# Kernel tuning notes

Hardware: AMD Instinct MI355X
Metric: run time of the kernel (lower is better)

Reference implementation:

```python
import jax, jax.numpy as jnp
import numpy as np

N = 50000        # nodes
E = 150000       # edges (avg degree ~3, chain-like RNA graphs)
F_IN = 32        # n_features
H = 32           # hidden_dim
C = 13           # n_classes
L = 3            # n_conv_layers
EDGE_HID = 10    # edge-net hidden width (Linear(2,10))
BN_EPS = 1e-5
SLOPE = 0.01     # leaky_relu default negative slope


def setup_inputs() -> dict:
    key = jax.random.key(0)
    ks = jax.random.split(key, 8)
    s = 0.1
    x = jax.random.normal(ks[0], (N, F_IN), dtype=jnp.float32)
    edge_index = jax.random.randint(ks[1], (2, E), 0, N)
    edge_attr = jax.random.uniform(ks[2], (E, 2), dtype=jnp.float32)
    # per-layer NNConv params stacked on a leading L axis (F_IN == H so all layers share shapes)
    netW1 = jax.random.normal(ks[3], (L, 2, EDGE_HID), dtype=jnp.float32) * s
    netb1 = jnp.zeros((L, EDGE_HID), dtype=jnp.float32)
    netW2 = jax.random.normal(ks[4], (L, EDGE_HID, F_IN * H), dtype=jnp.float32) * (s / np.sqrt(EDGE_HID).astype(np.float32))
    netb2 = jnp.zeros((L, F_IN * H), dtype=jnp.float32)
    root = jax.random.normal(ks[5], (L, F_IN, H), dtype=jnp.float32) * s
    conv_bias = jnp.zeros((L, H), dtype=jnp.float32)
    bn_gamma = jnp.ones((L, H), dtype=jnp.float32)
    bn_beta = jnp.zeros((L, H), dtype=jnp.float32)
    fcW = jax.random.normal(ks[6], (H, C), dtype=jnp.float32) * s
    fcb = jnp.zeros((C,), dtype=jnp.float32)
    return {"x": x, "edge_index": edge_index, "edge_attr": edge_attr,
            "netW1": netW1, "netb1": netb1, "netW2": netW2, "netb2": netb2,
            "root": root, "conv_bias": conv_bias,
            "bn_gamma": bn_gamma, "bn_beta": bn_beta, "fcW": fcW, "fcb": fcb}


def reference(x, edge_index, edge_attr, netW1, netb1, netW2, netb2, root,
              conv_bias, bn_gamma, bn_beta, fcW, fcb):
    src, dst = edge_index[0], edge_index[1]
    n = x.shape[0]
    h = x
    for i in range(L):
        # NNConv: per-edge weight matrix from edge MLP
        e = jax.nn.relu(edge_attr @ netW1[i] + netb1[i])            # [E, EDGE_HID]
        w = (e @ netW2[i] + netb2[i]).reshape(-1, h.shape[1], H)    # [E, in, H]
        m = jnp.einsum('ei,eio->eo', h[src], w)                     # messages [E, H]
        agg = jax.ops.segment_sum(m, dst, num_segments=n)           # scatter-add to targets
        h = agg + h @ root[i] + conv_bias[i]
        # BatchNorm1d (training-mode batch statistics)
        mu = h.mean(axis=0)
        var = h.var(axis=0)
        h = (h - mu) * jax.lax.rsqrt(var + BN_EPS) * bn_gamma[i] + bn_beta[i]
        # leaky_relu; dropout=0 is identity
        h = jnp.where(h > 0, h, SLOPE * h)
    logits = h @ fcW + fcb
    return jax.nn.log_softmax(logits, axis=1)
```

## Files before the change

### kernel.cpp

```cpp
#include <hip/hip_runtime.h>

#define NN 50000
#define EE 150000
#define BN_EPS 1e-5f
#define SLOPE 0.01f
#define SCAN_B 196
#define AGG_B  782
#define MSG_B  2344
#define CAP    344

typedef __attribute__((ext_vector_type(8))) short bf16x8;
typedef __attribute__((ext_vector_type(4))) float f32x4;

__global__ __launch_bounds__(256) void k_count(const int* __restrict__ ei, int* __restrict__ cnt) {
    int e = blockIdx.x * blockDim.x + threadIdx.x;
    if (e < EE) atomicAdd(&cnt[ei[EE + e]], 1);
}

__global__ __launch_bounds__(256) void k_scanA(const int* __restrict__ cnt,
                                               int* __restrict__ rowptr,
                                               int* __restrict__ bsum) {
    __shared__ int buf[256];
    int t = threadIdx.x;
    int idx = blockIdx.x * 256 + t;
    int v = (idx <= NN) ? cnt[idx] : 0;
    buf[t] = v;
    __syncthreads();
    for (int off = 1; off < 256; off <<= 1) {
        int add = (t >= off) ? buf[t - off] : 0;
        __syncthreads();
        buf[t] += add;
        __syncthreads();
    }
    if (idx <= NN) rowptr[idx] = buf[t] - v;
    if (t == 255) bsum[blockIdx.x] = buf[255];
}

__global__ __launch_bounds__(256) void k_scanB(int* __restrict__ bsum) {
    __shared__ int buf[256];
    int t = threadIdx.x;
    int v = (t < SCAN_B) ? bsum[t] : 0;
    buf[t] = v;
    __syncthreads();
    for (int off = 1; off < 256; off <<= 1) {
        int add = (t >= off) ? buf[t - off] : 0;
        __syncthreads();
        buf[t] += add;
        __syncthreads();
    }
    if (t < SCAN_B) bsum[t] = buf[t] - v;
}

__global__ __launch_bounds__(256) void k_scanC(int* __restrict__ rowptr,
                                               int* __restrict__ cursor,
                                               const int* __restrict__ bsum) {
    int idx = blockIdx.x * 256 + threadIdx.x;
    if (idx <= NN) {
        int r = rowptr[idx] + bsum[blockIdx.x];
        rowptr[idx] = r;
        cursor[idx] = r;
    }
}

__global__ __launch_bounds__(256) void k_fill(const int* __restrict__ ei,
                                              int* __restrict__ cursor,
                                              int* __restrict__ perm) {
    int e = blockIdx.x * blockDim.x + threadIdx.x;
    if (e < EE) perm[e] = atomicAdd(&cursor[ei[EE + e]], 1);
}

__global__ __launch_bounds__(256) void k_wprep(const float* __restrict__ netW2,
                                               const float* __restrict__ netb2,
                                               unsigned* __restrict__ Wfz) {
    int layer = blockIdx.y;
    int idx = blockIdx.x * 256 + threadIdx.x;
    if (idx >= 5632) return;
    const float* W2 = netW2 + layer * 10240;
    const float* b2 = netb2 + layer * 1024;
    int frag = idx >> 8;
    int rem  = idx & 255;
    int lane = rem >> 2;
    int j0   = (rem & 3) * 2;
    int tile = frag & 1;
    int kstep = frag >> 1;
    int o  = tile * 16 + (lane & 15);
    int kk = kstep * 32 + (lane >> 4) * 8 + j0;
    float v0, v1;
    if (kk < 320) {
        int base = (kk >> 5) * 1024 + (kk & 31) * 32 + o;
        v0 = W2[base];
        v1 = W2[base + 32];
    } else {
        int base = (kk - 320) * 32 + o;
        v0 = b2[base];
        v1 = b2[base + 32];
    }
    Wfz[layer * 5632 + idx] =
        __builtin_amdgcn_perm(__float_as_uint(v1), __float_as_uint(v0), 0x07060302u);
}

__device__ __forceinline__ void bn_scsh(const float* __restrict__ stats,
                                        const float* __restrict__ gamma,
                                        const float* __restrict__ beta,
                                        int flag, float* sc, float* sh) {
    if (flag && threadIdx.x < 32) {
        int o = threadIdx.x;
        float mu = stats[o] * (1.0f / NN);
        float var = stats[32 + o] * (1.0f / NN) - mu * mu;
        float s = gamma[o] * rsqrtf(var + BN_EPS);
        sc[o] = s;
        sh[o] = fmaf(-mu, s, beta[o]);
    }
}

__global__ __launch_bounds__(256) void k_msg(
    const float* __restrict__ h, const int* __restrict__ ei,
    const float* __restrict__ ea, const float* __restrict__ W1,
    const float* __restrict__ b1, const unsigned* __restrict__ Wfz,
    const float* __restrict__ stats, const float* __restrict__ gamma,
    const float* __restrict__ beta, int flag,
    const int* __restrict__ perm, float* __restrict__ m)
{
    int t = threadIdx.x;
    int lane = t & 63;
    int w = t >> 6;
    int col = lane & 15;
    int chunk = lane >> 4;
    int e = blockIdx.x * 64 + w * 16 + col;
    bool ev = e < EE;
    int s = ev ? ei[e] : 0;
    float2 a = ev ? ((const float2*)ea)[e] : make_float2(0.f, 0.f);

    float hv[8];
    *(float4*)&hv[0] = *(const float4*)(h + s * 32 + chunk * 8);
    *(float4*)&hv[4] = *(const float4*)(h + s * 32 + chunk * 8 + 4);

    if (flag) {
        int i0 = chunk * 8;
#pragma unroll
        for (int j = 0; j < 8; ++j) {
            int ch = i0 + j;
            float mu = stats[ch] * (1.0f / NN);
            float var = stats[32 + ch] * (1.0f / NN) - mu * mu;
            float scv = gamma[ch] * rsqrtf(var + BN_EPS);
            float shv = fmaf(-mu, scv, beta[ch]);
            float y = fmaf(hv[j], scv, shv);
            hv[j] = y > 0.f ? y : SLOPE * y;
        }
    }

    float ekv[11];
#pragma unroll
    for (int k = 0; k < 10; ++k)
        ekv[k] = fmaxf(fmaf(a.x, W1[k], fmaf(a.y, W1[10 + k], b1[k])), 0.0f);
    ekv[10] = 1.0f;

    f32x4 acc0 = {0.f, 0.f, 0.f, 0.f};
    f32x4 acc1 = {0.f, 0.f, 0.f, 0.f};
#pragma unroll
    for (int k = 0; k < 11; ++k) {
        float ekk = ekv[k];
        union { unsigned u[4]; bf16x8 v; } B;
        B.u[0] = __builtin_amdgcn_perm(__float_as_uint(ekk * hv[1]), __float_as_uint(ekk * hv[0]), 0x07060302u);
        B.u[1] = __builtin_amdgcn_perm(__float_as_uint(ekk * hv[3]), __float_as_uint(ekk * hv[2]), 0x07060302u);
        B.u[2] = __builtin_amdgcn_perm(__float_as_uint(ekk * hv[5]), __float_as_uint(ekk * hv[4]), 0x07060302u);
        B.u[3] = __builtin_amdgcn_perm(__float_as_uint(ekk * hv[7]), __float_as_uint(ekk * hv[6]), 0x07060302u);
        bf16x8 A0 = *(const bf16x8*)(Wfz + (k * 2)     * 256 + lane * 4);
        bf16x8 A1 = *(const bf16x8*)(Wfz + (k * 2 + 1) * 256 + lane * 4);
        acc0 = __builtin_amdgcn_mfma_f32_16x16x32_bf16(A0, B.v, acc0, 0, 0, 0);
        acc1 = __builtin_amdgcn_mfma_f32_16x16x32_bf16(A1, B.v, acc1, 0, 0, 0);
    }

    if (ev) {
        int p = perm[e];
        int r = chunk * 4;
        *(f32x4*)(m + (size_t)p * 32 + r)      = acc0;
        *(f32x4*)(m + (size_t)p * 32 + 16 + r) = acc1;
    }
}

__global__ __launch_bounds__(512) void k_agg(
    const float* __restrict__ h, const float* __restrict__ m,
    const int* __restrict__ rowptr,
    const float* __restrict__ root, const float* __restrict__ bias,
    const float* __restrict__ stats_prev, const float* __restrict__ gamma,
    const float* __restrict__ beta, int flag,
    float* __restrict__ hpre, float* __restrict__ stats_out)
{
    __shared__ float smb[CAP * 36];
    __shared__ float sc[32], sh[32];
    __shared__ float ls[2][8][8][4];

    bn_scsh(stats_prev, gamma, beta, flag, sc, sh);

    int t = threadIdx.x;
    int v0 = blockIdx.x * 64;
    int vend = v0 + 64 < NN ? v0 + 64 : NN;
    int p_start = rowptr[v0];
    int span = rowptr[vend] - p_start;
    int nstage = span < CAP ? span : CAP;

    for (int idx = t; idx < nstage * 8; idx += 512) {
        int r = idx >> 3, j = idx & 7;
        *(float4*)&smb[r * 36 + j * 4] = ((const float4*)m)[(size_t)(p_start + r) * 8 + j];
    }
    __syncthreads();

    int v = v0 + (t >> 3);
    int cg = t & 7;
    float4 acc = make_float4(0.f, 0.f, 0.f, 0.f);

    if (v < NN) {
        float hn[32];
        const float4* hp = (const float4*)(h + v * 32);
#pragma unroll
        for (int q = 0; q < 8; ++q) {
            float4 tt = hp[q];
            hn[4 * q] = tt.x; hn[4 * q + 1] = tt.y; hn[4 * q + 2] = tt.z; hn[4 * q + 3] = tt.w;
        }
        if (flag) {
#pragma unroll
            for (int i = 0; i < 32; ++i) {
                float y = fmaf(hn[i], sc[i], sh[i]);
                hn[i] = y > 0.f ? y : SLOPE * y;
            }
        }
        acc = ((const float4*)bias)[cg];
#pragma unroll
        for (int i = 0; i < 32; ++i) {
            float4 r = ((const float4*)(root + i * 32))[cg];
            acc.x = fmaf(hn[i], r.x, acc.x);
            acc.y = fmaf(hn[i], r.y, acc.y);
            acc.z = fmaf(hn[i], r.z, acc.z);
            acc.w = fmaf(hn[i], r.w, acc.w);
        }
        int q0 = rowptr[v] - p_start, q1 = rowptr[v + 1] - p_start;
        for (int p = q0; p < q1; ++p) {
            float4 tt;
            if (p < CAP) tt = *(const float4*)&smb[p * 36 + cg * 4];
            else         tt = ((const float4*)m)[(size_t)(p_start + p) * 8 + cg];
            acc.x += tt.x; acc.y += tt.y; acc.z += tt.z; acc.w += tt.w;
        }
        ((float4*)(hpre + v * 32))[cg] = acc;
    }

    float ss[8] = { acc.x, acc.y, acc.z, acc.w,
                    acc.x * acc.x, acc.y * acc.y, acc.z * acc.z, acc.w * acc.w };
#pragma unroll
    for (int d = 8; d < 64; d <<= 1) {
#pragma unroll
        for (int j = 0; j < 8; ++j) ss[j] += __shfl_xor(ss[j], d);
    }
    int wave = t >> 6, lane = t & 63;
    if (lane < 8) {
#pragma unroll
        for (int j = 0; j < 4; ++j) {
            ls[0][wave][lane][j] = ss[j];
            ls[1][wave][lane][j] = ss[4 + j];
        }
    }
    __syncthreads();
    if (t < 64) {
        int stat = t >> 5, idx = t & 31;
        int cgg = idx >> 2, ch = idx & 3;
        float val = 0.f;
#pragma unroll
        for (int wv = 0; wv < 8; ++wv) val += ls[stat][wv][cgg][ch];
        unsafeAtomicAdd(&stats_out[stat * 32 + idx], val);
    }
}

__global__ __launch_bounds__(256) void k_logits(const float* __restrict__ h,
                                                const float* __restrict__ fcW,
                                                const float* __restrict__ fcb,
                                                const float* __restrict__ stats,
                                                const float* __restrict__ gamma,
                                                const float* __restrict__ beta,
                                                float* __restrict__ out) {
    __shared__ float sc[32], sh[32];
    bn_scsh(stats, gamma, beta, 1, sc, sh);
    __syncthreads();

    int v = blockIdx.x * blockDim.x + threadIdx.x;
    if (v >= NN) return;
    float hv[32];
    const float4* hp = (const float4*)(h + v * 32);
#pragma unroll
    for (int q = 0; q < 8; ++q) {
        float4 t = hp[q];
        hv[4 * q] = t.x; hv[4 * q + 1] = t.y; hv[4 * q + 2] = t.z; hv[4 * q + 3] = t.w;
    }
#pragma unroll
    for (int i = 0; i < 32; ++i) {
        float y = fmaf(hv[i], sc[i], sh[i]);
        hv[i] = y > 0.f ? y : SLOPE * y;
    }
    float lg[13];
#pragma unroll
    for (int c = 0; c < 13; ++c) lg[c] = fcb[c];
#pragma unroll
    for (int i = 0; i < 32; ++i) {
        float z = hv[i];
#pragma unroll
        for (int c = 0; c < 13; ++c) lg[c] = fmaf(z, fcW[i * 13 + c], lg[c]);
    }
    float mx = lg[0];
#pragma unroll
    for (int c = 1; c < 13; ++c) mx = fmaxf(mx, lg[c]);
    float sum = 0.0f;
#pragma unroll
    for (int c = 0; c < 13; ++c) sum += expf(lg[c] - mx);
    float lse = mx + logf(sum);
#pragma unroll
    for (int c = 0; c < 13; ++c) out[v * 13 + c] = lg[c] - lse;
}

extern "C" void kernel_launch(void* const* d_in, const int* in_sizes, int n_in,
                              void* d_out, int out_size, void* d_ws, size_t ws_size,
                              hipStream_t stream) {
    const float* x     = (const float*)d_in[0];
    const int*   ei    = (const int*)  d_in[1];
    const float* ea    = (const float*)d_in[2];
    const float* netW1 = (const float*)d_in[3];
    const float* netb1 = (const float*)d_in[4];
    const float* netW2 = (const float*)d_in[5];
    const float* netb2 = (const float*)d_in[6];
    const float* root  = (const float*)d_in[7];
    const float* cbias = (const float*)d_in[8];
    const float* gamma = (const float*)d_in[9];
    const float* beta  = (const float*)d_in[10];
    const float* fcW   = (const float*)d_in[11];
    const float* fcb   = (const float*)d_in[12];
    float* out = (float*)d_out;

    char* w = (char*)d_ws;
    float*    m      = (float*)   (w);
    float*    hA     = (float*)   (w + 19200000);
    float*    hB     = (float*)   (w + 25600000);
    int*      rowptr = (int*)     (w + 32000000);
    int*      cursor = (int*)     (w + 32200064);
    int*      perm   = (int*)     (w + 32400128);
    float*    stats  = (float*)   (w + 33000128);
    int*      bsum   = (int*)     (w + 33000896);
    unsigned* Wfz    = (unsigned*)(w + 33001920);
    int*      cnt    = (int*)w;

    hipMemsetAsync(cnt, 0, (NN + 1) * sizeof(int), stream);
    hipMemsetAsync(stats, 0, 768, stream);

    k_wprep<<<dim3(22, 3), 256, 0, stream>>>(netW2, netb2, Wfz);
    k_count<<<(EE + 255) / 256, 256, 0, stream>>>(ei, cnt);
    k_scanA<<<SCAN_B, 256, 0, stream>>>(cnt, rowptr, bsum);
    k_scanB<<<1, 256, 0, stream>>>(bsum);
    k_scanC<<<SCAN_B, 256, 0, stream>>>(rowptr, cursor, bsum);
    k_fill <<<(EE + 255) / 256, 256, 0, stream>>>(ei, cursor, perm);

    const float* hcur = x;
    float* bufs[2] = { hA, hB };
    for (int i = 0; i < 3; ++i) {
        float* hnext = bufs[i & 1];
        const float* stprev = stats + (i - 1) * 64;
        k_msg<<<MSG_B, 256, 0, stream>>>(
            hcur, ei, ea, netW1 + i * 20, netb1 + i * 10, Wfz + i * 5632,
            stprev, gamma + (i - 1) * 32, beta + (i - 1) * 32, i > 0, perm, m);
        k_agg<<<AGG_B, 512, 0, stream>>>(
            hcur, m, rowptr, root + i * 1024, cbias + i * 32,
            stprev, gamma + (i - 1) * 32, beta + (i - 1) * 32, i > 0,
            hnext, stats + i * 64);
        hcur = hnext;
    }
    k_logits<<<(NN + 255) / 256, 256, 0, stream>>>(
        hcur, fcW, fcb, stats + 2 * 64, gamma + 2 * 32, beta + 2 * 32, out);
}
```

Before: 257.4 us.

## Fuse message computation into aggregation kernel via dst-sorted edge ids

Replaces the separate per-edge message kernel and per-node aggregation kernel with one per-layer kernel. Each block handles 64 destination nodes, walks their incoming edges through a dst-sorted edge-id list, computes messages with MFMA straight into shared memory in CAP-sized chunks, then reduces them. This removes the global round-trip of the E×32 message buffer and one launch per layer. In exchange the edge work is tied to the node blocking, which adds a barrier per chunk, gives uneven work across blocks, and reads h[src] and edge data indirectly through eids.

```diff
diff --git a/kernel.cpp b/kernel.cpp
--- a/kernel.cpp
+++ b/kernel.cpp
@@ -6,7 +6,6 @@
 #define SLOPE 0.01f
 #define SCAN_B 196
 #define AGG_B  782
-#define MSG_B  2344
 #define CAP    344
 
 typedef __attribute__((ext_vector_type(8))) short bf16x8;
@@ -64,9 +63,12 @@
 
 __global__ __launch_bounds__(256) void k_fill(const int* __restrict__ ei,
                                               int* __restrict__ cursor,
-                                              int* __restrict__ perm) {
+                                              int* __restrict__ eids) {
     int e = blockIdx.x * blockDim.x + threadIdx.x;
-    if (e < EE) perm[e] = atomicAdd(&cursor[ei[EE + e]], 1);
+    if (e < EE) {
+        int pos = atomicAdd(&cursor[ei[EE + e]], 1);
+        eids[pos] = e;
+    }
 }
 
 __global__ __launch_bounds__(256) void k_wprep(const float* __restrict__ netW2,
@@ -113,75 +115,11 @@
     }
 }
 
-__global__ __launch_bounds__(256) void k_msg(
+__global__ __launch_bounds__(512) void k_layer(
     const float* __restrict__ h, const int* __restrict__ ei,
     const float* __restrict__ ea, const float* __restrict__ W1,
     const float* __restrict__ b1, const unsigned* __restrict__ Wfz,
-    const float* __restrict__ stats, const float* __restrict__ gamma,
-    const float* __restrict__ beta, int flag,
-    const int* __restrict__ perm, float* __restrict__ m)
-{
-    int t = threadIdx.x;
-    int lane = t & 63;
-    int w = t >> 6;
-    int col = lane & 15;
-    int chunk = lane >> 4;
-    int e = blockIdx.x * 64 + w * 16 + col;
-    bool ev = e < EE;
-    int s = ev ? ei[e] : 0;
-    float2 a = ev ? ((const float2*)ea)[e] : make_float2(0.f, 0.f);
-
-    float hv[8];
-    *(float4*)&hv[0] = *(const float4*)(h + s * 32 + chunk * 8);
-    *(float4*)&hv[4] = *(const float4*)(h + s * 32 + chunk * 8 + 4);
-
-    if (flag) {
-        int i0 = chunk * 8;
-#pragma unroll
-        for (int j = 0; j < 8; ++j) {
-            int ch = i0 + j;
-            float mu = stats[ch] * (1.0f / NN);
-            float var = stats[32 + ch] * (1.0f / NN) - mu * mu;
-            float scv = gamma[ch] * rsqrtf(var + BN_EPS);
-            float shv = fmaf(-mu, scv, beta[ch]);
-            float y = fmaf(hv[j], scv, shv);
-            hv[j] = y > 0.f ? y : SLOPE * y;
-        }
-    }
-
-    float ekv[11];
-#pragma unroll
-    for (int k = 0; k < 10; ++k)
-        ekv[k] = fmaxf(fmaf(a.x, W1[k], fmaf(a.y, W1[10 + k], b1[k])), 0.0f);
-    ekv[10] = 1.0f;
-
-    f32x4 acc0 = {0.f, 0.f, 0.f, 0.f};
-    f32x4 acc1 = {0.f, 0.f, 0.f, 0.f};
-#pragma unroll
-    for (int k = 0; k < 11; ++k) {
-        float ekk = ekv[k];
-        union { unsigned u[4]; bf16x8 v; } B;
-        B.u[0] = __builtin_amdgcn_perm(__float_as_uint(ekk * hv[1]), __float_as_uint(ekk * hv[0]), 0x07060302u);
-        B.u[1] = __builtin_amdgcn_perm(__float_as_uint(ekk * hv[3]), __float_as_uint(ekk * hv[2]), 0x07060302u);
-        B.u[2] = __builtin_amdgcn_perm(__float_as_uint(ekk * hv[5]), __float_as_uint(ekk * hv[4]), 0x07060302u);
-        B.u[3] = __builtin_amdgcn_perm(__float_as_uint(ekk * hv[7]), __float_as_uint(ekk * hv[6]), 0x07060302u);
-        bf16x8 A0 = *(const bf16x8*)(Wfz + (k * 2)     * 256 + lane * 4);
-        bf16x8 A1 = *(const bf16x8*)(Wfz + (k * 2 + 1) * 256 + lane * 4);
-        acc0 = __builtin_amdgcn_mfma_f32_16x16x32_bf16(A0, B.v, acc0, 0, 0, 0);
-        acc1 = __builtin_amdgcn_mfma_f32_16x16x32_bf16(A1, B.v, acc1, 0, 0, 0);
-    }
-
-    if (ev) {
-        int p = perm[e];
-        int r = chunk * 4;
-        *(f32x4*)(m + (size_t)p * 32 + r)      = acc0;
-        *(f32x4*)(m + (size_t)p * 32 + 16 + r) = acc1;
-    }
-}
-
-__global__ __launch_bounds__(512) void k_agg(
-    const float* __restrict__ h, const float* __restrict__ m,
-    const int* __restrict__ rowptr,
+    const int* __restrict__ rowptr, const int* __restrict__ eids,
     const float* __restrict__ root, const float* __restrict__ bias,
     const float* __restrict__ stats_prev, const float* __restrict__ gamma,
     const float* __restrict__ beta, int flag,
@@ -191,20 +129,14 @@
     __shared__ float sc[32], sh[32];
     __shared__ float ls[2][8][8][4];
 
+    int t = threadIdx.x;
     bn_scsh(stats_prev, gamma, beta, flag, sc, sh);
-
-    int t = threadIdx.x;
+    __syncthreads();
+
     int v0 = blockIdx.x * 64;
     int vend = v0 + 64 < NN ? v0 + 64 : NN;
     int p_start = rowptr[v0];
     int span = rowptr[vend] - p_start;
-    int nstage = span < CAP ? span : CAP;
-
-    for (int idx = t; idx < nstage * 8; idx += 512) {
-        int r = idx >> 3, j = idx & 7;
-        *(float4*)&smb[r * 36 + j * 4] = ((const float4*)m)[(size_t)(p_start + r) * 8 + j];
-    }
-    __syncthreads();
 
     int v = v0 + (t >> 3);
     int cg = t & 7;
@@ -234,15 +166,78 @@
             acc.z = fmaf(hn[i], r.z, acc.z);
             acc.w = fmaf(hn[i], r.w, acc.w);
         }
-        int q0 = rowptr[v] - p_start, q1 = rowptr[v + 1] - p_start;
-        for (int p = q0; p < q1; ++p) {
-            float4 tt;
-            if (p < CAP) tt = *(const float4*)&smb[p * 36 + cg * 4];
-            else         tt = ((const float4*)m)[(size_t)(p_start + p) * 8 + cg];
-            acc.x += tt.x; acc.y += tt.y; acc.z += tt.z; acc.w += tt.w;
-        }
-        ((float4*)(hpre + v * 32))[cg] = acc;
-    }
+    }
+
+    int lane = t & 63;
+    int w = t >> 6;
+    int col = lane & 15;
+    int chunk = lane >> 4;
+
+    for (int c0 = 0; c0 < span; c0 += CAP) {
+        int csize = span - c0 < CAP ? span - c0 : CAP;
+
+        for (int base = 0; base < csize; base += 128) {
+            int sl = base + w * 16 + col;
+            bool evv = sl < csize;
+            int e = evv ? eids[p_start + c0 + sl] : 0;
+            int s = evv ? ei[e] : 0;
+            float2 a = evv ? ((const float2*)ea)[e] : make_float2(0.f, 0.f);
+
+            float hv[8];
+            *(float4*)&hv[0] = *(const float4*)(h + s * 32 + chunk * 8);
+            *(float4*)&hv[4] = *(const float4*)(h + s * 32 + chunk * 8 + 4);
+            if (flag) {
+                int i0 = chunk * 8;
+#pragma unroll
+                for (int j = 0; j < 8; ++j) {
+                    float y = fmaf(hv[j], sc[i0 + j], sh[i0 + j]);
+                    hv[j] = y > 0.f ? y : SLOPE * y;
+                }
+            }
+
+            float ekv[11];
+#pragma unroll
+            for (int k = 0; k < 10; ++k)
+                ekv[k] = fmaxf(fmaf(a.x, W1[k], fmaf(a.y, W1[10 + k], b1[k])), 0.0f);
+            ekv[10] = 1.0f;
+
+            f32x4 acc0 = {0.f, 0.f, 0.f, 0.f};
+            f32x4 acc1 = {0.f, 0.f, 0.f, 0.f};
+#pragma unroll
+            for (int k = 0; k < 11; ++k) {
+                float ekk = ekv[k];
+                union { unsigned u[4]; bf16x8 v; } B;
+                B.u[0] = __builtin_amdgcn_perm(__float_as_uint(ekk * hv[1]), __float_as_uint(ekk * hv[0]), 0x07060302u);
+                B.u[1] = __builtin_amdgcn_perm(__float_as_uint(ekk * hv[3]), __float_as_uint(ekk * hv[2]), 0x07060302u);
+                B.u[2] = __builtin_amdgcn_perm(__float_as_uint(ekk * hv[5]), __float_as_uint(ekk * hv[4]), 0x07060302u);
+                B.u[3] = __builtin_amdgcn_perm(__float_as_uint(ekk * hv[7]), __float_as_uint(ekk * hv[6]), 0x07060302u);
+                bf16x8 A0 = *(const bf16x8*)(Wfz + (k * 2)     * 256 + lane * 4);
+                bf16x8 A1 = *(const bf16x8*)(Wfz + (k * 2 + 1) * 256 + lane * 4);
+                acc0 = __builtin_amdgcn_mfma_f32_16x16x32_bf16(A0, B.v, acc0, 0, 0, 0);
+                acc1 = __builtin_amdgcn_mfma_f32_16x16x32_bf16(A1, B.v, acc1, 0, 0, 0);
+            }
+
+            if (evv) {
+                *(f32x4*)&smb[sl * 36 + chunk * 4]      = acc0;
+                *(f32x4*)&smb[sl * 36 + 16 + chunk * 4] = acc1;
+            }
+        }
+        __syncthreads();
+
+        if (v < NN) {
+            int q0 = rowptr[v] - p_start - c0;
+            int q1 = rowptr[v + 1] - p_start - c0;
+            q0 = q0 > 0 ? q0 : 0;
+            q1 = q1 < csize ? q1 : csize;
+            for (int p = q0; p < q1; ++p) {
+                float4 tt = *(const float4*)&smb[p * 36 + cg * 4];
+                acc.x += tt.x; acc.y += tt.y; acc.z += tt.z; acc.w += tt.w;
+            }
+        }
+        __syncthreads();
+    }
+
+    if (v < NN) ((float4*)(hpre + v * 32))[cg] = acc;
 
     float ss[8] = { acc.x, acc.y, acc.z, acc.w,
                     acc.x * acc.x, acc.y * acc.y, acc.z * acc.z, acc.w * acc.w };
@@ -251,12 +246,12 @@
 #pragma unroll
         for (int j = 0; j < 8; ++j) ss[j] += __shfl_xor(ss[j], d);
     }
-    int wave = t >> 6, lane = t & 63;
-    if (lane < 8) {
+    int wave = t >> 6, lane2 = t & 63;
+    if (lane2 < 8) {
 #pragma unroll
         for (int j = 0; j < 4; ++j) {
-            ls[0][wave][lane][j] = ss[j];
-            ls[1][wave][lane][j] = ss[4 + j];
+            ls[0][wave][lane2][j] = ss[j];
+            ls[1][wave][lane2][j] = ss[4 + j];
         }
     }
     __syncthreads();
@@ -334,16 +329,15 @@
     float* out = (float*)d_out;
 
     char* w = (char*)d_ws;
-    float*    m      = (float*)   (w);
-    float*    hA     = (float*)   (w + 19200000);
-    float*    hB     = (float*)   (w + 25600000);
-    int*      rowptr = (int*)     (w + 32000000);
-    int*      cursor = (int*)     (w + 32200064);
-    int*      perm   = (int*)     (w + 32400128);
-    float*    stats  = (float*)   (w + 33000128);
-    int*      bsum   = (int*)     (w + 33000896);
-    unsigned* Wfz    = (unsigned*)(w + 33001920);
-    int*      cnt    = (int*)w;
+    float*    hA     = (float*)   (w);
+    float*    hB     = (float*)   (w +  6400000);
+    int*      rowptr = (int*)     (w + 12800000);
+    int*      cursor = (int*)     (w + 13000064);
+    int*      eids   = (int*)     (w + 13200128);
+    float*    stats  = (float*)   (w + 13800128);
+    int*      bsum   = (int*)     (w + 13800896);
+    unsigned* Wfz    = (unsigned*)(w + 13801920);
+    int*      cnt    = (int*)     (w + 13869504);
 
     hipMemsetAsync(cnt, 0, (NN + 1) * sizeof(int), stream);
     hipMemsetAsync(stats, 0, 768, stream);
@@ -353,18 +347,16 @@
     k_scanA<<<SCAN_B, 256, 0, stream>>>(cnt, rowptr, bsum);
     k_scanB<<<1, 256, 0, stream>>>(bsum);
     k_scanC<<<SCAN_B, 256, 0, stream>>>(rowptr, cursor, bsum);
-    k_fill <<<(EE + 255) / 256, 256, 0, stream>>>(ei, cursor, perm);
+    k_fill <<<(EE + 255) / 256, 256, 0, stream>>>(ei, cursor, eids);
 
     const float* hcur = x;
     float* bufs[2] = { hA, hB };
     for (int i = 0; i < 3; ++i) {
         float* hnext = bufs[i & 1];
         const float* stprev = stats + (i - 1) * 64;
-        k_msg<<<MSG_B, 256, 0, stream>>>(
+        k_layer<<<AGG_B, 512, 0, stream>>>(
             hcur, ei, ea, netW1 + i * 20, netb1 + i * 10, Wfz + i * 5632,
-            stprev, gamma + (i - 1) * 32, beta + (i - 1) * 32, i > 0, perm, m);
-        k_agg<<<AGG_B, 512, 0, stream>>>(
-            hcur, m, rowptr, root + i * 1024, cbias + i * 32,
+            rowptr, eids, root + i * 1024, cbias + i * 32,
             stprev, gamma + (i - 1) * 32, beta + (i - 1) * 32, i > 0,
             hnext, stats + i * 64);
         hcur = hnext;
```

New measurement: 253.0 us. About the same (-1.7%).
